# Kernel optimization log

Measured on AMD Instinct MI355X. Metric: run time of the kernel, lower is better.

Reference implementation:

```python
import jax, jax.numpy as jnp
import numpy as np
from jax import lax

I_CH = 3
C_CH = 2 * I_CH            # 6
PAIRS = [(i, j) for i in range(C_CH) for j in range(i + 1, C_CH)]  # 15 Givens pairs


def _encoder(x, W, b_enc):
    # CMEncoder stand-in: single SAME 3x3 conv in_channels -> out_channels
    y = lax.conv_general_dilated(x, W, (1, 1), 'SAME',
                                 dimension_numbers=('NCHW', 'OIHW', 'NCHW'))
    return y + b_enc[None, :, None, None]


def _covariance_matrix(s, a):
    # s: [b,C,h,w] per-pixel variances; a: [b,15,h,w] Givens angles
    d = jnp.moveaxis(s, 1, -1)      # [b,h,w,C]
    ang = jnp.moveaxis(a, 1, -1)    # [b,h,w,15]
    b, h, w, Cc = d.shape
    R = jnp.broadcast_to(jnp.eye(Cc, dtype=d.dtype), (b, h, w, Cc, Cc))
    for k, (i, j) in enumerate(PAIRS):
        c = jnp.cos(ang[..., k])[..., None]
        sn = jnp.sin(ang[..., k])[..., None]
        ci = R[..., :, i]
        cj = R[..., :, j]
        R = R.at[..., :, i].set(c * ci + sn * cj)
        R = R.at[..., :, j].set(-sn * ci + c * cj)
    # S = R diag(d) R^T  -> [b,h,w,C,C]
    S = jnp.einsum('bhwmk,bhwk,bhwnk->bhwmn', R, d, R)
    return S, R, d


def reference(x, W, b_enc):
    I = I_CH
    C = C_CH
    p = _encoder(x, W, b_enc)              # [b,30,h,w]
    m = p[:, :C]                           # means [b,6,h,w]
    s = p[:, C:2 * C]
    s = jnp.square(jax.nn.relu(s) - jax.nn.relu(-s))
    s = jnp.clip(s, 1e-6)
    a = 2.0 * jnp.pi * jax.nn.sigmoid(p[:, 2 * C:-I])
    xf = p[:, -I:]                         # [b,3,h,w]
    S, R, d = _covariance_matrix(s, a)
    # S^{-1} = R diag(1/d) R^T (D diagonal, R orthogonal) -> [b,h,w,6,6]
    S_1 = jnp.einsum('bhwmk,bhwk,bhwnk->bhwmn', R, 1.0 / d, R)
    Sxx = S_1[..., :I, :I]
    Syx = S_1[..., I:, :I]
    Q = jnp.matmul(Syx, jnp.linalg.inv(Sxx))   # [b,h,w,3,3]
    mx = m[:, :I]
    my = m[:, I:]
    y = my + jnp.einsum('bijmn,bnij->bmij', Q, xf - mx)
    Sout = jnp.transpose(S, (0, 3, 4, 1, 2))   # [b,6,6,h,w]
    return (xf, m, Sout, y)


def setup_inputs() -> dict:
    key = jax.random.key(0)
    k1, k2, k3 = jax.random.split(key, 3)
    x = jax.random.normal(k1, (4, 3, 256, 256), dtype=jnp.float32)
    W = jax.random.normal(k2, (30, 3, 3, 3), dtype=jnp.float32) * 0.1
    b_enc = jax.random.normal(k3, (30,), dtype=jnp.float32) * 0.1
    return {'x': x, 'W': W, 'b_enc': b_enc}
```

## Files before the change

### kernel.cpp

```cpp
#include <hip/hip_runtime.h>
#include <math.h>

#define HWp 65536

typedef float v2f __attribute__((ext_vector_type(2)));

__device__ __forceinline__ v2f fma2(v2f a, v2f b, v2f c) {
    return __builtin_elementwise_fma(a, b, c);
}

__global__ __launch_bounds__(128)
void gp_encoder_kernel(const float* __restrict__ x,
                       const float* __restrict__ Wt,
                       const float* __restrict__ be,
                       float* __restrict__ out)
{
    __shared__ float Rsh[64][38];

    const int lane = threadIdx.x & 63;
    const int wid  = threadIdx.x >> 6;

    const int blk  = blockIdx.x;
    const int b    = blk >> 10;
    const int pixb = (blk & 1023) << 6;
    const int h    = pixb >> 8;
    const int w0   = pixb & 255;

    const bool wlo_ok = !(w0 == 0   && lane == 0);
    const bool whi_ok = !(w0 == 192 && lane == 63);
    const int  idx_m1 = wlo_ok ? lane - 1 : lane;
    const int  idx_p1 = whi_ok ? lane + 1 : lane;

    float xs[27];
    const float* xb = x + b * 3 * HWp;
    #pragma unroll
    for (int ci = 0; ci < 3; ++ci) {
        #pragma unroll
        for (int kh = 0; kh < 3; ++kh) {
            const int hh = h + kh - 1;
            float v0 = 0.f, v1 = 0.f, v2 = 0.f;
            if ((unsigned)hh < 256u) {
                const float* rp = xb + ci * HWp + hh * 256 + w0;
                v0 = rp[idx_m1];
                v1 = rp[lane];
                v2 = rp[idx_p1];
                v0 = wlo_ok ? v0 : 0.f;
                v2 = whi_ok ? v2 : 0.f;
            }
            xs[ci*9 + kh*3 + 0] = v0;
            xs[ci*9 + kh*3 + 1] = v1;
            xs[ci*9 + kh*3 + 2] = v2;
        }
    }
    v2f xp[13];
    #pragma unroll
    for (int q = 0; q < 13; ++q)
        xp[q] = (v2f){xs[2*q], xs[2*q + 1]};
    const float x26 = xs[26];

    float* out_xf = out                      + b*3*HWp  + pixb;
    float* out_m  = out + 4*3*HWp            + b*6*HWp  + pixb;
    float* out_S  = out + (4*3+4*6)*HWp      + b*36*HWp + pixb;
    float* out_y  = out + (4*3+4*6+4*36)*HWp + b*3*HWp  + pixb;

    float pb[15];
    v2f   d2[3];

    if (wid == 0) {
        float pa[15];
        #pragma unroll
        for (int o = 0; o < 15; ++o) {
            const int base = (12 + o) * 27;
            v2f acc2 = (v2f){0.f, 0.f};
            #pragma unroll
            for (int q = 0; q < 13; ++q) {
                v2f wq;
                wq.x = Wt[base + 2*q];
                wq.y = Wt[base + 2*q + 1];
                acc2 = fma2(xp[q], wq, acc2);
            }
            const float r = be[12 + o] + acc2.x + acc2.y;
            pa[o] = fmaf(x26, Wt[base + 26], r);
        }

        float cs[15], ss[15];
        #pragma unroll
        for (int k = 0; k < 15; ++k) {
            const float e  = __expf(-pa[k]);
            const float sg = __builtin_amdgcn_rcpf(1.f + e);
            cs[k] = __builtin_amdgcn_cosf(sg);
            ss[k] = __builtin_amdgcn_sinf(sg);
        }

        v2f Rc[6][3];
        #pragma unroll
        for (int c = 0; c < 6; ++c)
            #pragma unroll
            for (int p = 0; p < 3; ++p)
                Rc[c][p] = (v2f){(2*p == c) ? 1.f : 0.f, (2*p + 1 == c) ? 1.f : 0.f};

        const int PI_[15] = {0,0,0,0,0,1,1,1,1,2,2,2,3,3,4};
        const int PJ_[15] = {1,2,3,4,5,2,3,4,5,3,4,5,4,5,5};
        #pragma unroll
        for (int k = 0; k < 15; ++k) {
            const int i = PI_[k], j = PJ_[k];
            const v2f c2 = (v2f){cs[k], cs[k]};
            const v2f s2 = (v2f){ss[k], ss[k]};
            #pragma unroll
            for (int p = 0; p < 3; ++p) {
                const v2f ri = Rc[i][p], rj = Rc[j][p];
                Rc[i][p] = fma2(c2, ri, s2 * rj);
                Rc[j][p] = fma2(c2, rj, -(s2 * ri));
            }
        }

        #pragma unroll
        for (int m = 0; m < 6; ++m)
            #pragma unroll
            for (int k = 0; k < 6; ++k)
                Rsh[lane][m*6 + k] = (m & 1) ? Rc[k][m >> 1].y : Rc[k][m >> 1].x;
    } else {
        #pragma unroll
        for (int o = 0; o < 15; ++o) {
            const int ch   = (o < 12) ? o : (o + 15);
            const int base = ch * 27;
            v2f acc2 = (v2f){0.f, 0.f};
            #pragma unroll
            for (int q = 0; q < 13; ++q) {
                v2f wq;
                wq.x = Wt[base + 2*q];
                wq.y = Wt[base + 2*q + 1];
                acc2 = fma2(xp[q], wq, acc2);
            }
            const float r = be[ch] + acc2.x + acc2.y;
            pb[o] = fmaf(x26, Wt[base + 26], r);
        }

        #pragma unroll
        for (int c = 0; c < 6; ++c)
            out_m[c*HWp + lane] = pb[c];
        #pragma unroll
        for (int i = 0; i < 3; ++i)
            out_xf[i*HWp + lane] = pb[12 + i];

        #pragma unroll
        for (int p = 0; p < 3; ++p) {
            const v2f s = (v2f){pb[6 + 2*p], pb[7 + 2*p]};
            d2[p] = __builtin_elementwise_max(s * s, (v2f){1e-6f, 1e-6f});
        }
    }

    __syncthreads();

    if (wid == 0) return;

    v2f R2[6][3];
    #pragma unroll
    for (int m = 0; m < 6; ++m)
        #pragma unroll
        for (int p = 0; p < 3; ++p)
            R2[m][p] = *reinterpret_cast<const v2f*>(&Rsh[lane][m*6 + 2*p]);

    float syxf[3][3], syyf[3][3];
    #pragma unroll
    for (int m = 0; m < 6; ++m) {
        v2f rdm[3];
        #pragma unroll
        for (int p = 0; p < 3; ++p)
            rdm[p] = R2[m][p] * d2[p];
        #pragma unroll
        for (int n = m; n < 6; ++n) {
            v2f a2 = rdm[0] * R2[n][0];
            a2 = fma2(rdm[1], R2[n][1], a2);
            a2 = fma2(rdm[2], R2[n][2], a2);
            const float acc = a2.x + a2.y;
            out_S[(m*6 + n)*HWp + lane] = acc;
            if (n != m)
                out_S[(n*6 + m)*HWp + lane] = acc;
            if (m < 3) { if (n >= 3) syxf[n-3][m] = acc; }
            else       { syyf[m-3][n-3] = acc; if (n != m) syyf[n-3][m-3] = acc; }
        }
    }

    const double a00 = (double)syyf[0][0], a01 = (double)syyf[0][1], a02 = (double)syyf[0][2];
    const double a10 = (double)syyf[1][0], a11 = (double)syyf[1][1], a12 = (double)syyf[1][2];
    const double a20 = (double)syyf[2][0], a21 = (double)syyf[2][1], a22 = (double)syyf[2][2];

    const double det = a00*(a11*a22 - a12*a21)
                     - a01*(a10*a22 - a12*a20)
                     + a02*(a10*a21 - a11*a20);
    const double idet = 1.0 / det;

    double inv[3][3];
    inv[0][0] =  (a11*a22 - a12*a21) * idet;
    inv[0][1] = -(a01*a22 - a02*a21) * idet;
    inv[0][2] =  (a01*a12 - a02*a11) * idet;
    inv[1][0] = -(a10*a22 - a12*a20) * idet;
    inv[1][1] =  (a00*a22 - a02*a20) * idet;
    inv[1][2] = -(a00*a12 - a02*a10) * idet;
    inv[2][0] =  (a10*a21 - a11*a20) * idet;
    inv[2][1] = -(a00*a21 - a01*a20) * idet;
    inv[2][2] =  (a00*a11 - a01*a10) * idet;

    double Qp[3][3];
    #pragma unroll
    for (int r = 0; r < 3; ++r)
        #pragma unroll
        for (int c = 0; c < 3; ++c) {
            double acc = 0.0;
            #pragma unroll
            for (int k = 0; k < 3; ++k)
                acc = fma(inv[r][k], (double)syxf[k][c], acc);
            Qp[r][c] = acc;
        }

    #pragma unroll
    for (int i = 0; i < 3; ++i) {
        double acc = (double)pb[3 + i];
        #pragma unroll
        for (int n = 0; n < 3; ++n)
            acc = fma(-Qp[i][n], (double)pb[12 + n] - (double)pb[n], acc);
        out_y[i*HWp + lane] = (float)acc;
    }
}

extern "C" void kernel_launch(void* const* d_in, const int* in_sizes, int n_in,
                              void* d_out, int out_size, void* d_ws, size_t ws_size,
                              hipStream_t stream) {
    const float* x  = (const float*)d_in[0];
    const float* Wt = (const float*)d_in[1];
    const float* be = (const float*)d_in[2];
    float* out = (float*)d_out;

    dim3 grid(4096);
    dim3 block(128);
    hipLaunchKernelGGL(gp_encoder_kernel, grid, block, 0, stream, x, Wt, be, out);
}
```

Measured before the change: 23.94 us.

## Rebalance work so wave 0 computes covariance and wave 1 solves Q

Instead of wave 0 handing R to wave 1 through shared memory and then sitting idle, wave 1 now sends the diagonal variances to wave 0. Wave 0 builds S = R diag(d) R^T, writes all 36 S outputs, and passes back the 18 entries needed for Syx and Syy. Wave 1 then does the double-precision 3x3 inverse and the y output. This spreads the post-barrier work across both waves and shrinks shared memory, at the cost of a second barrier and a computation order that differs from the old symmetric reuse. Launch bounds also request 6 blocks per CU.

```diff
diff --git a/kernel.cpp b/kernel.cpp
--- a/kernel.cpp
+++ b/kernel.cpp
@@ -9,13 +9,14 @@
     return __builtin_elementwise_fma(a, b, c);
 }
 
-__global__ __launch_bounds__(128)
+__global__ __launch_bounds__(128, 6)
 void gp_encoder_kernel(const float* __restrict__ x,
                        const float* __restrict__ Wt,
                        const float* __restrict__ be,
                        float* __restrict__ out)
 {
-    __shared__ float Rsh[64][38];
+    __shared__ float Dsh[6][64];
+    __shared__ float Ssh[18][64];
 
     const int lane = threadIdx.x & 63;
     const int wid  = threadIdx.x >> 6;
@@ -64,7 +65,6 @@
     float* out_y  = out + (4*3+4*6+4*36)*HWp + b*3*HWp  + pixb;
 
     float pb[15];
-    v2f   d2[3];
 
     if (wid == 0) {
         float pa[15];
@@ -83,29 +83,24 @@
             pa[o] = fmaf(x26, Wt[base + 26], r);
         }
 
-        float cs[15], ss[15];
+        v2f Rc[6][3];
+        #pragma unroll
+        for (int c = 0; c < 6; ++c)
+            #pragma unroll
+            for (int p = 0; p < 3; ++p)
+                Rc[c][p] = (v2f){(2*p == c) ? 1.f : 0.f, (2*p + 1 == c) ? 1.f : 0.f};
+
+        const int PI_[15] = {0,0,0,0,0,1,1,1,1,2,2,2,3,3,4};
+        const int PJ_[15] = {1,2,3,4,5,2,3,4,5,3,4,5,4,5,5};
         #pragma unroll
         for (int k = 0; k < 15; ++k) {
+            const int i = PI_[k], j = PJ_[k];
             const float e  = __expf(-pa[k]);
             const float sg = __builtin_amdgcn_rcpf(1.f + e);
-            cs[k] = __builtin_amdgcn_cosf(sg);
-            ss[k] = __builtin_amdgcn_sinf(sg);
-        }
-
-        v2f Rc[6][3];
-        #pragma unroll
-        for (int c = 0; c < 6; ++c)
-            #pragma unroll
-            for (int p = 0; p < 3; ++p)
-                Rc[c][p] = (v2f){(2*p == c) ? 1.f : 0.f, (2*p + 1 == c) ? 1.f : 0.f};
-
-        const int PI_[15] = {0,0,0,0,0,1,1,1,1,2,2,2,3,3,4};
-        const int PJ_[15] = {1,2,3,4,5,2,3,4,5,3,4,5,4,5,5};
-        #pragma unroll
-        for (int k = 0; k < 15; ++k) {
-            const int i = PI_[k], j = PJ_[k];
-            const v2f c2 = (v2f){cs[k], cs[k]};
-            const v2f s2 = (v2f){ss[k], ss[k]};
+            const float c  = __builtin_amdgcn_cosf(sg);
+            const float sn = __builtin_amdgcn_sinf(sg);
+            const v2f c2 = (v2f){c, c};
+            const v2f s2 = (v2f){sn, sn};
             #pragma unroll
             for (int p = 0; p < 3; ++p) {
                 const v2f ri = Rc[i][p], rj = Rc[j][p];
@@ -114,11 +109,41 @@
             }
         }
 
-        #pragma unroll
-        for (int m = 0; m < 6; ++m)
-            #pragma unroll
-            for (int k = 0; k < 6; ++k)
-                Rsh[lane][m*6 + k] = (m & 1) ? Rc[k][m >> 1].y : Rc[k][m >> 1].x;
+        __syncthreads();
+
+        float dk[6];
+        #pragma unroll
+        for (int k = 0; k < 6; ++k)
+            dk[k] = Dsh[k][lane];
+
+        #pragma unroll
+        for (int n = 0; n < 6; ++n) {
+            float t[6];
+            #pragma unroll
+            for (int k = 0; k < 6; ++k) {
+                const float rnk = (n & 1) ? Rc[k][n >> 1].y : Rc[k][n >> 1].x;
+                t[k] = dk[k] * rnk;
+            }
+            v2f col[3];
+            #pragma unroll
+            for (int p = 0; p < 3; ++p) {
+                v2f acc = Rc[0][p] * (v2f){t[0], t[0]};
+                #pragma unroll
+                for (int k = 1; k < 6; ++k)
+                    acc = fma2(Rc[k][p], (v2f){t[k], t[k]}, acc);
+                col[p] = acc;
+            }
+            #pragma unroll
+            for (int p = 0; p < 3; ++p) {
+                out_S[((2*p    )*6 + n)*HWp + lane] = col[p].x;
+                out_S[((2*p + 1)*6 + n)*HWp + lane] = col[p].y;
+            }
+            Ssh[n*3 + 0][lane] = col[1].y;
+            Ssh[n*3 + 1][lane] = col[2].x;
+            Ssh[n*3 + 2][lane] = col[2].y;
+        }
+
+        __syncthreads();
     } else {
         #pragma unroll
         for (int o = 0; o < 15; ++o) {
@@ -144,83 +169,63 @@
             out_xf[i*HWp + lane] = pb[12 + i];
 
         #pragma unroll
-        for (int p = 0; p < 3; ++p) {
-            const v2f s = (v2f){pb[6 + 2*p], pb[7 + 2*p]};
-            d2[p] = __builtin_elementwise_max(s * s, (v2f){1e-6f, 1e-6f});
-        }
-    }
-
-    __syncthreads();
-
-    if (wid == 0) return;
-
-    v2f R2[6][3];
-    #pragma unroll
-    for (int m = 0; m < 6; ++m)
-        #pragma unroll
-        for (int p = 0; p < 3; ++p)
-            R2[m][p] = *reinterpret_cast<const v2f*>(&Rsh[lane][m*6 + 2*p]);
-
-    float syxf[3][3], syyf[3][3];
-    #pragma unroll
-    for (int m = 0; m < 6; ++m) {
-        v2f rdm[3];
-        #pragma unroll
-        for (int p = 0; p < 3; ++p)
-            rdm[p] = R2[m][p] * d2[p];
-        #pragma unroll
-        for (int n = m; n < 6; ++n) {
-            v2f a2 = rdm[0] * R2[n][0];
-            a2 = fma2(rdm[1], R2[n][1], a2);
-            a2 = fma2(rdm[2], R2[n][2], a2);
-            const float acc = a2.x + a2.y;
-            out_S[(m*6 + n)*HWp + lane] = acc;
-            if (n != m)
-                out_S[(n*6 + m)*HWp + lane] = acc;
-            if (m < 3) { if (n >= 3) syxf[n-3][m] = acc; }
-            else       { syyf[m-3][n-3] = acc; if (n != m) syyf[n-3][m-3] = acc; }
-        }
-    }
-
-    const double a00 = (double)syyf[0][0], a01 = (double)syyf[0][1], a02 = (double)syyf[0][2];
-    const double a10 = (double)syyf[1][0], a11 = (double)syyf[1][1], a12 = (double)syyf[1][2];
-    const double a20 = (double)syyf[2][0], a21 = (double)syyf[2][1], a22 = (double)syyf[2][2];
-
-    const double det = a00*(a11*a22 - a12*a21)
-                     - a01*(a10*a22 - a12*a20)
-                     + a02*(a10*a21 - a11*a20);
-    const double idet = 1.0 / det;
-
-    double inv[3][3];
-    inv[0][0] =  (a11*a22 - a12*a21) * idet;
-    inv[0][1] = -(a01*a22 - a02*a21) * idet;
-    inv[0][2] =  (a01*a12 - a02*a11) * idet;
-    inv[1][0] = -(a10*a22 - a12*a20) * idet;
-    inv[1][1] =  (a00*a22 - a02*a20) * idet;
-    inv[1][2] = -(a00*a12 - a02*a10) * idet;
-    inv[2][0] =  (a10*a21 - a11*a20) * idet;
-    inv[2][1] = -(a00*a21 - a01*a20) * idet;
-    inv[2][2] =  (a00*a11 - a01*a10) * idet;
-
-    double Qp[3][3];
-    #pragma unroll
-    for (int r = 0; r < 3; ++r)
-        #pragma unroll
-        for (int c = 0; c < 3; ++c) {
-            double acc = 0.0;
-            #pragma unroll
-            for (int k = 0; k < 3; ++k)
-                acc = fma(inv[r][k], (double)syxf[k][c], acc);
-            Qp[r][c] = acc;
-        }
-
-    #pragma unroll
-    for (int i = 0; i < 3; ++i) {
-        double acc = (double)pb[3 + i];
-        #pragma unroll
-        for (int n = 0; n < 3; ++n)
-            acc = fma(-Qp[i][n], (double)pb[12 + n] - (double)pb[n], acc);
-        out_y[i*HWp + lane] = (float)acc;
+        for (int k = 0; k < 6; ++k) {
+            const float s = pb[6 + k];
+            Dsh[k][lane] = fmaxf(s * s, 1e-6f);
+        }
+
+        __syncthreads();
+        __syncthreads();
+
+        float syxf[3][3], syyf[3][3];
+        #pragma unroll
+        for (int c = 0; c < 3; ++c)
+            #pragma unroll
+            for (int r = 0; r < 3; ++r) {
+                syxf[r][c] = Ssh[c*3 + r][lane];
+                syyf[r][c] = Ssh[(3 + c)*3 + r][lane];
+            }
+
+        const double a00 = (double)syyf[0][0], a01 = (double)syyf[0][1], a02 = (double)syyf[0][2];
+        const double a10 = (double)syyf[1][0], a11 = (double)syyf[1][1], a12 = (double)syyf[1][2];
+        const double a20 = (double)syyf[2][0], a21 = (double)syyf[2][1], a22 = (double)syyf[2][2];
+
+        const double det = a00*(a11*a22 - a12*a21)
+                         - a01*(a10*a22 - a12*a20)
+                         + a02*(a10*a21 - a11*a20);
+        const double idet = 1.0 / det;
+
+        double inv[3][3];
+        inv[0][0] =  (a11*a22 - a12*a21) * idet;
+        inv[0][1] = -(a01*a22 - a02*a21) * idet;
+        inv[0][2] =  (a01*a12 - a02*a11) * idet;
+        inv[1][0] = -(a10*a22 - a12*a20) * idet;
+        inv[1][1] =  (a00*a22 - a02*a20) * idet;
+        inv[1][2] = -(a00*a12 - a02*a10) * idet;
+        inv[2][0] =  (a10*a21 - a11*a20) * idet;
+        inv[2][1] = -(a00*a21 - a01*a20) * idet;
+        inv[2][2] =  (a00*a11 - a01*a10) * idet;
+
+        double Qp[3][3];
+        #pragma unroll
+        for (int r = 0; r < 3; ++r)
+            #pragma unroll
+            for (int c = 0; c < 3; ++c) {
+                double acc = 0.0;
+                #pragma unroll
+                for (int k = 0; k < 3; ++k)
+                    acc = fma(inv[r][k], (double)syxf[k][c], acc);
+                Qp[r][c] = acc;
+            }
+
+        #pragma unroll
+        for (int i = 0; i < 3; ++i) {
+            double acc = (double)pb[3 + i];
+            #pragma unroll
+            for (int n = 0; n < 3; ++n)
+                acc = fma(-Qp[i][n], (double)pb[12 + n] - (double)pb[n], acc);
+            out_y[i*HWp + lane] = (float)acc;
+        }
     }
 }
 
```

After: 23.99 us. Within noise of the previous version (+0.2%).
